# Optimization experiments

Hardware: AMD Instinct MI355X
Metric: run time of the kernel (lower is better)

Reference implementation:

```python
import jax, jax.numpy as jnp
import numpy as np

D_MODEL = 1024
NUM_HEADS = 16
D_K = D_MODEL // NUM_HEADS
B, S = 2, 2048


def setup_inputs() -> dict:
    key = jax.random.key(0)
    ks = jax.random.split(key, 9)
    scale = 1.0 / np.sqrt(D_MODEL)
    return {
        "hidden_states": jax.random.normal(ks[0], (B, S, D_MODEL), dtype=jnp.float32),
        "attention_mask": jnp.ones((B, S, S), dtype=jnp.int32),
        "Wq": jax.random.normal(ks[1], (D_MODEL, D_MODEL), dtype=jnp.float32) * scale,
        "bq": jnp.zeros((D_MODEL,), dtype=jnp.float32),
        "Wk": jax.random.normal(ks[2], (D_MODEL, D_MODEL), dtype=jnp.float32) * scale,
        "bk": jnp.zeros((D_MODEL,), dtype=jnp.float32),
        "Wv": jax.random.normal(ks[3], (D_MODEL, D_MODEL), dtype=jnp.float32) * scale,
        "bv": jnp.zeros((D_MODEL,), dtype=jnp.float32),
        "Wo": jax.random.normal(ks[4], (D_MODEL, D_MODEL), dtype=jnp.float32) * scale,
        "bo": jnp.zeros((D_MODEL,), dtype=jnp.float32),
    }


def reference(hidden_states, attention_mask, Wq, bq, Wk, bk, Wv, bv, Wo, bo):
    b, s, _ = hidden_states.shape
    # torch Linear: y = x @ W.T + b
    def proj(W, bias):
        y = jnp.einsum('bsd,ed->bse', hidden_states, W) + bias
        return y.reshape(b, s, NUM_HEADS, D_K).transpose(0, 2, 1, 3)  # [B,H,S,dk]
    q = proj(Wq, bq)
    k = proj(Wk, bk)
    v = proj(Wv, bv)
    scores = jnp.einsum('bnqd,bnkd->bnqk', q, k) / np.sqrt(D_K)
    mask = attention_mask[:, None, :, :]  # [B,1,S,S]
    scores = jnp.where(mask == 0, jnp.float32(-1e9), scores)
    attn = jax.nn.softmax(scores, axis=-1)  # dropout = identity (eval)
    ctx = jnp.einsum('bnqk,bnkd->bnqd', attn, v)
    ctx = ctx.transpose(0, 2, 1, 3).reshape(b, s, D_MODEL)
    return jnp.einsum('bsd,ed->bse', ctx, Wo) + bo
```

## Files before the change

kernel.cpp:

```cpp
#include <hip/hip_runtime.h>

typedef short short8 __attribute__((ext_vector_type(8)));
typedef float floatx4 __attribute__((ext_vector_type(4)));
typedef float floatx16 __attribute__((ext_vector_type(16)));
typedef unsigned short ushort4v __attribute__((ext_vector_type(4)));

#define DEV static __device__ __forceinline__

DEV unsigned short f2bf(float f) {
  unsigned int u = __builtin_bit_cast(unsigned int, f);
  u += 0x7fffu + ((u >> 16) & 1u);
  return (unsigned short)(u >> 16);
}

DEV unsigned int cvtpk(float a, float b) {
  unsigned int r;
  asm("v_cvt_pk_bf16_f32 %0, %1, %2" : "=v"(r) : "v"(a), "v"(b));
  return r;
}

DEV void gload16(const unsigned short* g, unsigned short* l) {
  __builtin_amdgcn_global_load_lds((__attribute__((address_space(1))) void*)g,
                                   (__attribute__((address_space(3))) void*)l,
                                   16, 0, 0);
}

__global__ void convert_kernel(const float* __restrict__ hs, const float* __restrict__ Wq,
                               const float* __restrict__ Wk, const float* __restrict__ Wv,
                               const float* __restrict__ Wo,
                               unsigned short* __restrict__ xbf, unsigned short* __restrict__ wqkv,
                               unsigned short* __restrict__ wobf,
                               const int* __restrict__ mask, unsigned long long* __restrict__ bits) {
  if (blockIdx.x >= 8192) {
    int w = (blockIdx.x - 8192) * 256 + threadIdx.x;
    const int4* p = (const int4*)(mask + (size_t)w * 64);
    unsigned long long r = 0ull;
#pragma unroll
    for (int j = 0; j < 16; ++j) {
      int4 m = p[j];
      r |= (unsigned long long)(m.x != 0) << (j * 4 + 0);
      r |= (unsigned long long)(m.y != 0) << (j * 4 + 1);
      r |= (unsigned long long)(m.z != 0) << (j * 4 + 2);
      r |= (unsigned long long)(m.w != 0) << (j * 4 + 3);
    }
    bits[w] = r;
    return;
  }
  size_t i4 = ((size_t)blockIdx.x * 256 + threadIdx.x) * 4;
  const float* src;
  unsigned short* dst;
  if (i4 < 4194304) {
    const int r = (int)(i4 >> 10), c = (int)(i4 & 1023);
    src = hs + i4;
    const int p = r >> 6, fi = (r & 63) >> 4, l15f = r & 15;
    const int ktc = c >> 5, qdc = (c >> 3) & 3, e = c & 7;
    dst = xbf + ((size_t)(p * 128 + ktc * 4 + fi) * 512 + (qdc * 16 + l15f) * 8 + e);
  } else if (i4 < 7340032) {
    size_t o = i4 - 4194304;
    size_t lo = o & 1048575;
    src = (o < 1048576) ? (Wq + lo) : ((o < 2097152) ? (Wk + lo) : (Wv + lo));
    const int r = (int)(o >> 10), c = (int)(o & 1023);
    const int p = r >> 6, fi = (r & 63) >> 4, l15f = r & 15;
    const int ktc = c >> 5, qdc = (c >> 3) & 3, e = c & 7;
    dst = wqkv + ((size_t)(p * 128 + ktc * 4 + fi) * 512 + (qdc * 16 + l15f) * 8 + e);
  } else {
    size_t o = i4 - 7340032;
    src = Wo + o; dst = wobf + o;
  }
  float4 v = *(const float4*)src;
  ushort4v u;
  u.x = f2bf(v.x); u.y = f2bf(v.y); u.z = f2bf(v.z); u.w = f2bf(v.w);
  *(ushort4v*)dst = u;
}

__global__ void __launch_bounds__(256, 2) qkv_gemm(
    const unsigned short* __restrict__ Xf, const unsigned short* __restrict__ Wf,
    const float* __restrict__ bq, const float* __restrict__ bk, const float* __restrict__ bv,
    unsigned short* __restrict__ Qb, unsigned short* __restrict__ Kb,
    unsigned short* __restrict__ Vt) {
  const int tid = threadIdx.x;
  const int lane = tid & 63, wv = tid >> 6;
  const int wm = wv >> 1, wn = wv & 1;
  const int quad = lane >> 4, l15 = lane & 15;
  const int mb = blockIdx.y, nb = blockIdx.x;
  const bool sw = (nb < 16);

  const int wx = sw ? wn : wm;
  const int ww = sw ? wm : wn;

  const unsigned short* xp = Xf + (size_t)(mb * 2 + wx) * 65536 + lane * 8;
  const unsigned short* wp = Wf + (size_t)(nb * 2 + ww) * 65536 + lane * 8;

  short8 xa[4], wb[4];
#pragma unroll
  for (int i = 0; i < 4; ++i) xa[i] = *(const short8*)(xp + i * 512);
#pragma unroll
  for (int i = 0; i < 4; ++i) wb[i] = *(const short8*)(wp + i * 512);

  floatx4 acc[4][4] = {};
  for (int kt = 0; kt < 32; ++kt) {
    if (sw) {
#pragma unroll
      for (int mt = 0; mt < 4; ++mt)
#pragma unroll
        for (int nt = 0; nt < 4; ++nt)
          acc[mt][nt] = __builtin_amdgcn_mfma_f32_16x16x32_bf16(wb[mt], xa[nt], acc[mt][nt], 0, 0, 0);
    } else {
#pragma unroll
      for (int mt = 0; mt < 4; ++mt)
#pragma unroll
        for (int nt = 0; nt < 4; ++nt)
          acc[mt][nt] = __builtin_amdgcn_mfma_f32_16x16x32_bf16(xa[mt], wb[nt], acc[mt][nt], 0, 0, 0);
    }
    xp += 2048; wp += 2048;
    if (kt < 31) {
#pragma unroll
      for (int i = 0; i < 4; ++i) xa[i] = *(const short8*)(xp + i * 512);
#pragma unroll
      for (int i = 0; i < 4; ++i) wb[i] = *(const short8*)(wp + i * 512);
    }
  }

  if (sw) {
#pragma unroll
    for (int mt = 0; mt < 4; ++mt) {
      const int wc0 = nb * 128 + wm * 64 + mt * 16 + quad * 4;
      const int mat = wc0 >> 10;
      const int nl0 = wc0 & 1023;
      const int hh = nl0 >> 6, d0 = nl0 & 63;
      const float4 b4 = *(const float4*)((mat ? bk : bq) + nl0);
      const float fac = mat ? 1.0f : 0.18033688011112042f;
#pragma unroll
      for (int nt = 0; nt < 4; ++nt) {
        const int colx = mb * 128 + wn * 64 + nt * 16 + l15;
        const int bb = colx >> 11, s = colx & 2047;
        ushort4v pv;
        pv[0] = f2bf((acc[mt][nt][0] + b4.x) * fac);
        pv[1] = f2bf((acc[mt][nt][1] + b4.y) * fac);
        pv[2] = f2bf((acc[mt][nt][2] + b4.z) * fac);
        pv[3] = f2bf((acc[mt][nt][3] + b4.w) * fac);
        if (mat == 0) {
          *(ushort4v*)&Qb[((size_t)(bb * 16 + hh) * 2048 + s) * 64 + d0] = pv;
        } else {
          const size_t idx = (size_t)(bb * 16 + hh) * 131072 + (s >> 5) * 2048 +
                             (d0 >> 4) * 512 + (((d0 >> 3) & 1) * 32 + (s & 31)) * 8 + (d0 & 7);
          *(ushort4v*)&Kb[idx] = pv;
        }
      }
    }
  } else {
#pragma unroll
    for (int nt = 0; nt < 4; ++nt) {
      const int col = nb * 128 + wn * 64 + nt * 16 + l15;
      const int nl = col & 1023;
      const float bias = bv[nl];
      const int hh = nl >> 6, d = nl & 63;
#pragma unroll
      for (int mt = 0; mt < 4; ++mt) {
        const int row0 = mb * 128 + wm * 64 + mt * 16 + quad * 4;
        const int bb = row0 >> 11, s0 = row0 & 2047;
        ushort4v pv;
#pragma unroll
        for (int r = 0; r < 4; ++r) pv[r] = f2bf(acc[mt][nt][r] + bias);
        const size_t idx = (size_t)(bb * 16 + hh) * 131072 + (s0 >> 5) * 2048 +
                           ((s0 >> 4) & 1) * 1024 + (d >> 5) * 512 +
                           (((s0 >> 3) & 1) * 32 + (d & 31)) * 8 + (s0 & 7);
        *(ushort4v*)&Vt[idx] = pv;
      }
    }
  }
}

__global__ void __launch_bounds__(256, 2) attn_kernel(
    const unsigned short* __restrict__ Qb, const unsigned short* __restrict__ Kb,
    const unsigned short* __restrict__ Vt, const unsigned long long* __restrict__ mbits,
    unsigned short* __restrict__ ctx) {
  __shared__ float red[2 * 64 * 33];
  const int tid = threadIdx.x;
  const int lane = tid & 63, wv = tid >> 6;
  const int l31 = lane & 31, h = lane >> 5;
  const int qg = wv & 1, h2 = wv >> 1;
  const int bid = (blockIdx.x & 7) * 128 + (blockIdx.x >> 3);
  const int pair = bid >> 5, qt = bid & 31;
  const int b_ = pair >> 4, hd = pair & 15;
  const int qrow = qt * 64 + qg * 32 + l31;

  short8 qf[4];
#pragma unroll
  for (int ks = 0; ks < 4; ++ks)
    qf[ks] = *(const short8*)(Qb + (size_t)pair * 131072 + (size_t)qrow * 64 + ks * 16 + h * 8);

  const unsigned short* kp = Kb + (size_t)pair * 131072 + h2 * 65536 + lane * 8;
  const unsigned short* vp = Vt + (size_t)pair * 131072 + h2 * 65536 + lane * 8;

  const unsigned long long* mrow = mbits + ((size_t)b_ * 2048 + qrow) * 32 + h2 * 16;

  short8 kf[4], vf[4];
#pragma unroll
  for (int i = 0; i < 4; ++i) kf[i] = *(const short8*)(kp + i * 512);
#pragma unroll
  for (int i = 0; i < 4; ++i) vf[i] = *(const short8*)(vp + i * 512);

  floatx16 acc_o[2] = {};
  const floatx16 Zv = {};
  float lsum = 0.f;

#pragma unroll 2
  for (int it = 0; it < 32; ++it) {
    const unsigned long long w = mrow[it >> 1];
    const int bitbase = (it & 1) * 32;

    __builtin_amdgcn_s_setprio(1);
    floatx16 accs = __builtin_amdgcn_mfma_f32_32x32x16_bf16(kf[0], qf[0], Zv, 0, 0, 0);
#pragma unroll
    for (int ks = 1; ks < 4; ++ks)
      accs = __builtin_amdgcn_mfma_f32_32x32x16_bf16(kf[ks], qf[ks], accs, 0, 0, 0);
    __builtin_amdgcn_s_setprio(0);

    kp += 2048;
#pragma unroll
    for (int i = 0; i < 4; ++i) kf[i] = *(const short8*)(kp + i * 512);

    if (__any(w != ~0ull)) {
#pragma unroll
      for (int reg = 0; reg < 16; ++reg) {
        const int kl = (reg & 3) + 8 * (reg >> 2) + 4 * h;
        if (!((w >> (bitbase + kl)) & 1ull)) accs[reg] = -6e9f;
      }
    }

    unsigned int pk[8];
    float ls0 = 0.f, ls1 = 0.f;
#pragma unroll
    for (int i = 0; i < 8; ++i) {
      const float a = exp2f(accs[2 * i]);
      const float b = exp2f(accs[2 * i + 1]);
      ls0 += a;
      ls1 += b;
      pk[i] = cvtpk(a, b);
    }
    lsum += ls0 + ls1;
#pragma unroll
    for (int u = 0; u < 2; ++u) {
      auto r02 = __builtin_amdgcn_permlane32_swap(pk[4 * u + 0], pk[4 * u + 2], false, false);
      auto r13 = __builtin_amdgcn_permlane32_swap(pk[4 * u + 1], pk[4 * u + 3], false, false);
      union { unsigned int wd[4]; short8 s8; } af;
      af.wd[0] = r02[0];
      af.wd[1] = r13[0];
      af.wd[2] = r02[1];
      af.wd[3] = r13[1];
      __builtin_amdgcn_s_setprio(1);
#pragma unroll
      for (int nt = 0; nt < 2; ++nt)
        acc_o[nt] = __builtin_amdgcn_mfma_f32_32x32x16_bf16(af.s8, vf[u * 2 + nt], acc_o[nt], 0, 0, 0);
      __builtin_amdgcn_s_setprio(0);
    }

    vp += 2048;
#pragma unroll
    for (int i = 0; i < 4; ++i) vf[i] = *(const short8*)(vp + i * 512);
  }

  lsum += __shfl_xor(lsum, 32);

  if (h2 == 1) {
    float* p = red + (qg * 64 + lane) * 33;
#pragma unroll
    for (int reg = 0; reg < 16; ++reg) {
      p[reg] = acc_o[0][reg];
      p[16 + reg] = acc_o[1][reg];
    }
    p[32] = lsum;
  }
  __syncthreads();
  if (h2 == 0) {
    const float* p = red + (qg * 64 + lane) * 33;
#pragma unroll
    for (int reg = 0; reg < 16; ++reg) {
      acc_o[0][reg] += p[reg];
      acc_o[1][reg] += p[16 + reg];
    }
    lsum += p[32];
    const float rinv = 1.f / ((lsum > 0.f) ? lsum : 1.f);
#pragma unroll
    for (int reg = 0; reg < 16; ++reg) {
      const int ql = (reg & 3) + 8 * (reg >> 2) + 4 * h;
      const float rl = __shfl(rinv, ql);
      const size_t base = ((size_t)b_ * 2048 + qt * 64 + qg * 32 + ql) * 1024 + hd * 64;
      ctx[base + l31]      = f2bf(acc_o[0][reg] * rl);
      ctx[base + 32 + l31] = f2bf(acc_o[1][reg] * rl);
    }
  }
}

__global__ void __launch_bounds__(256, 2) out_gemm(
    const unsigned short* __restrict__ C, const unsigned short* __restrict__ W,
    const float* __restrict__ bo, float* __restrict__ out) {
  __shared__ __align__(16) unsigned short As[128 * 32];
  __shared__ __align__(16) unsigned short Bs[64 * 32];
  const int tid = threadIdx.x;
  const int lane = tid & 63, wv = tid >> 6;
  const int wm = wv >> 1, wn = wv & 1;
  const int quad = lane >> 4, l15 = lane & 15;
  const int mb = blockIdx.y, nb = blockIdx.x;

  const unsigned short* ga = C + (size_t)(mb * 128 + (tid >> 2)) * 1024 + (tid & 3) * 8;
  const unsigned short* gb = W + (size_t)(nb * 64 + (tid >> 2)) * 1024 + (tid & 3) * 8;
  unsigned short* la1 = As + tid * 8;
  unsigned short* la2 = As + 2048 + tid * 8;
  unsigned short* lb1 = Bs + tid * 8;

  floatx4 acc[4][2] = {};
  for (int kt = 0; kt < 32; ++kt) {
    const int k0 = kt * 32;
    gload16(ga + k0, la1);
    gload16(ga + k0 + 65536, la2);
    gload16(gb + k0, lb1);
    __syncthreads();
    short8 af[4], bfr[2];
#pragma unroll
    for (int i = 0; i < 4; ++i)
      af[i] = *(const short8*)&As[(wm * 64 + i * 16 + l15) * 32 + quad * 8];
#pragma unroll
    for (int i = 0; i < 2; ++i)
      bfr[i] = *(const short8*)&Bs[(wn * 32 + i * 16 + l15) * 32 + quad * 8];
#pragma unroll
    for (int mt = 0; mt < 4; ++mt)
#pragma unroll
      for (int nt = 0; nt < 2; ++nt)
        acc[mt][nt] = __builtin_amdgcn_mfma_f32_16x16x32_bf16(af[mt], bfr[nt], acc[mt][nt], 0, 0, 0);
    __syncthreads();
  }
#pragma unroll
  for (int nt = 0; nt < 2; ++nt) {
    const int col = nb * 64 + wn * 32 + nt * 16 + l15;
    const float bias = bo[col];
#pragma unroll
    for (int mt = 0; mt < 4; ++mt)
#pragma unroll
      for (int r = 0; r < 4; ++r) {
        const int row = mb * 128 + wm * 64 + mt * 16 + quad * 4 + r;
        out[(size_t)row * 1024 + col] = acc[mt][nt][r] + bias;
      }
  }
}

extern "C" void kernel_launch(void* const* d_in, const int* in_sizes, int n_in,
                              void* d_out, int out_size, void* d_ws, size_t ws_size,
                              hipStream_t stream) {
  const float* hs = (const float*)d_in[0];
  const int* mask = (const int*)d_in[1];
  const float* Wq = (const float*)d_in[2];
  const float* bq = (const float*)d_in[3];
  const float* Wk = (const float*)d_in[4];
  const float* bk = (const float*)d_in[5];
  const float* Wv = (const float*)d_in[6];
  const float* bv = (const float*)d_in[7];
  const float* Wo = (const float*)d_in[8];
  const float* bo = (const float*)d_in[9];
  float* out = (float*)d_out;

  char* ws = (char*)d_ws;
  unsigned short* xbf  = (unsigned short*)(ws + 0);
  unsigned short* wqkv = (unsigned short*)(ws + 8388608);
  unsigned short* wobf = (unsigned short*)(ws + 14680064);
  unsigned short* Qb   = (unsigned short*)(ws + 16777216);
  unsigned short* Kb   = (unsigned short*)(ws + 25165824);
  unsigned short* Vt   = (unsigned short*)(ws + 33554432);
  unsigned short* ctx  = (unsigned short*)(ws + 41943040);
  unsigned long long* mbits = (unsigned long long*)(ws + 50331648);

  convert_kernel<<<8704, 256, 0, stream>>>(hs, Wq, Wk, Wv, Wo, xbf, wqkv, wobf, mask, mbits);
  qkv_gemm<<<dim3(24, 32), 256, 0, stream>>>(xbf, wqkv, bq, bk, bv, Qb, Kb, Vt);
  attn_kernel<<<1024, 256, 0, stream>>>(Qb, Kb, Vt, mbits, ctx);
  out_gemm<<<dim3(16, 32), 256, 0, stream>>>(ctx, wobf, bo, out);
}
```

Baseline: 246.8 us.

## Store ctx and Wo in MFMA fragment layout; load out_gemm operands directly to registers

```diff
diff --git a/kernel.cpp b/kernel.cpp
--- a/kernel.cpp
+++ b/kernel.cpp
@@ -19,11 +19,6 @@
   return r;
 }
 
-DEV void gload16(const unsigned short* g, unsigned short* l) {
-  __builtin_amdgcn_global_load_lds((__attribute__((address_space(1))) void*)g,
-                                   (__attribute__((address_space(3))) void*)l,
-                                   16, 0, 0);
-}
 
 __global__ void convert_kernel(const float* __restrict__ hs, const float* __restrict__ Wq,
                                const float* __restrict__ Wk, const float* __restrict__ Wv,
@@ -49,24 +44,27 @@
   size_t i4 = ((size_t)blockIdx.x * 256 + threadIdx.x) * 4;
   const float* src;
   unsigned short* dst;
+  int r, c;
+  unsigned short* base;
   if (i4 < 4194304) {
-    const int r = (int)(i4 >> 10), c = (int)(i4 & 1023);
     src = hs + i4;
-    const int p = r >> 6, fi = (r & 63) >> 4, l15f = r & 15;
-    const int ktc = c >> 5, qdc = (c >> 3) & 3, e = c & 7;
-    dst = xbf + ((size_t)(p * 128 + ktc * 4 + fi) * 512 + (qdc * 16 + l15f) * 8 + e);
+    r = (int)(i4 >> 10); c = (int)(i4 & 1023);
+    base = xbf;
   } else if (i4 < 7340032) {
     size_t o = i4 - 4194304;
     size_t lo = o & 1048575;
     src = (o < 1048576) ? (Wq + lo) : ((o < 2097152) ? (Wk + lo) : (Wv + lo));
-    const int r = (int)(o >> 10), c = (int)(o & 1023);
-    const int p = r >> 6, fi = (r & 63) >> 4, l15f = r & 15;
-    const int ktc = c >> 5, qdc = (c >> 3) & 3, e = c & 7;
-    dst = wqkv + ((size_t)(p * 128 + ktc * 4 + fi) * 512 + (qdc * 16 + l15f) * 8 + e);
+    r = (int)(o >> 10); c = (int)(o & 1023);
+    base = wqkv;
   } else {
     size_t o = i4 - 7340032;
-    src = Wo + o; dst = wobf + o;
-  }
+    src = Wo + o;
+    r = (int)(o >> 10); c = (int)(o & 1023);
+    base = wobf;
+  }
+  const int p = r >> 6, fi = (r & 63) >> 4, l15f = r & 15;
+  const int ktc = c >> 5, qdc = (c >> 3) & 3, e = c & 7;
+  dst = base + ((size_t)(p * 128 + ktc * 4 + fi) * 512 + (qdc * 16 + l15f) * 8 + e);
   float4 v = *(const float4*)src;
   ushort4v u;
   u.x = f2bf(v.x); u.y = f2bf(v.y); u.z = f2bf(v.z); u.w = f2bf(v.w);
@@ -174,7 +172,7 @@
 __global__ void __launch_bounds__(256, 2) attn_kernel(
     const unsigned short* __restrict__ Qb, const unsigned short* __restrict__ Kb,
     const unsigned short* __restrict__ Vt, const unsigned long long* __restrict__ mbits,
-    unsigned short* __restrict__ ctx) {
+    unsigned short* __restrict__ ctxf) {
   __shared__ float red[2 * 64 * 33];
   const int tid = threadIdx.x;
   const int lane = tid & 63, wv = tid >> 6;
@@ -282,54 +280,53 @@
     }
     lsum += p[32];
     const float rinv = 1.f / ((lsum > 0.f) ? lsum : 1.f);
+    const size_t pbaseF = (size_t)(b_ * 32 + qt) * 65536;
+    const int qde = ((l31 >> 3) & 3) * 16;
+    const int e7 = l31 & 7;
 #pragma unroll
     for (int reg = 0; reg < 16; ++reg) {
       const int ql = (reg & 3) + 8 * (reg >> 2) + 4 * h;
       const float rl = __shfl(rinv, ql);
-      const size_t base = ((size_t)b_ * 2048 + qt * 64 + qg * 32 + ql) * 1024 + hd * 64;
-      ctx[base + l31]      = f2bf(acc_o[0][reg] * rl);
-      ctx[base + 32 + l31] = f2bf(acc_o[1][reg] * rl);
+      const int iq = qg * 2 + (ql >> 4);
+      const size_t off = (size_t)(qde + (ql & 15)) * 8 + e7;
+      ctxf[pbaseF + (size_t)((hd * 2) * 4 + iq) * 512 + off]     = f2bf(acc_o[0][reg] * rl);
+      ctxf[pbaseF + (size_t)((hd * 2 + 1) * 4 + iq) * 512 + off] = f2bf(acc_o[1][reg] * rl);
     }
   }
 }
 
 __global__ void __launch_bounds__(256, 2) out_gemm(
-    const unsigned short* __restrict__ C, const unsigned short* __restrict__ W,
+    const unsigned short* __restrict__ Cf, const unsigned short* __restrict__ Wof,
     const float* __restrict__ bo, float* __restrict__ out) {
-  __shared__ __align__(16) unsigned short As[128 * 32];
-  __shared__ __align__(16) unsigned short Bs[64 * 32];
   const int tid = threadIdx.x;
   const int lane = tid & 63, wv = tid >> 6;
   const int wm = wv >> 1, wn = wv & 1;
   const int quad = lane >> 4, l15 = lane & 15;
   const int mb = blockIdx.y, nb = blockIdx.x;
 
-  const unsigned short* ga = C + (size_t)(mb * 128 + (tid >> 2)) * 1024 + (tid & 3) * 8;
-  const unsigned short* gb = W + (size_t)(nb * 64 + (tid >> 2)) * 1024 + (tid & 3) * 8;
-  unsigned short* la1 = As + tid * 8;
-  unsigned short* la2 = As + 2048 + tid * 8;
-  unsigned short* lb1 = Bs + tid * 8;
+  const unsigned short* ap = Cf + (size_t)(mb * 2 + wm) * 65536 + lane * 8;
+  const unsigned short* bp = Wof + (size_t)nb * 65536 + (size_t)(wn * 2) * 512 + lane * 8;
+
+  short8 af[4], bfr[2];
+#pragma unroll
+  for (int i = 0; i < 4; ++i) af[i] = *(const short8*)(ap + i * 512);
+#pragma unroll
+  for (int i = 0; i < 2; ++i) bfr[i] = *(const short8*)(bp + i * 512);
 
   floatx4 acc[4][2] = {};
   for (int kt = 0; kt < 32; ++kt) {
-    const int k0 = kt * 32;
-    gload16(ga + k0, la1);
-    gload16(ga + k0 + 65536, la2);
-    gload16(gb + k0, lb1);
-    __syncthreads();
-    short8 af[4], bfr[2];
-#pragma unroll
-    for (int i = 0; i < 4; ++i)
-      af[i] = *(const short8*)&As[(wm * 64 + i * 16 + l15) * 32 + quad * 8];
-#pragma unroll
-    for (int i = 0; i < 2; ++i)
-      bfr[i] = *(const short8*)&Bs[(wn * 32 + i * 16 + l15) * 32 + quad * 8];
 #pragma unroll
     for (int mt = 0; mt < 4; ++mt)
 #pragma unroll
       for (int nt = 0; nt < 2; ++nt)
         acc[mt][nt] = __builtin_amdgcn_mfma_f32_16x16x32_bf16(af[mt], bfr[nt], acc[mt][nt], 0, 0, 0);
-    __syncthreads();
+    ap += 2048; bp += 2048;
+    if (kt < 31) {
+#pragma unroll
+      for (int i = 0; i < 4; ++i) af[i] = *(const short8*)(ap + i * 512);
+#pragma unroll
+      for (int i = 0; i < 2; ++i) bfr[i] = *(const short8*)(bp + i * 512);
+    }
   }
 #pragma unroll
   for (int nt = 0; nt < 2; ++nt) {
@@ -367,11 +364,11 @@
   unsigned short* Qb   = (unsigned short*)(ws + 16777216);
   unsigned short* Kb   = (unsigned short*)(ws + 25165824);
   unsigned short* Vt   = (unsigned short*)(ws + 33554432);
-  unsigned short* ctx  = (unsigned short*)(ws + 41943040);
+  unsigned short* ctxf = (unsigned short*)(ws + 41943040);
   unsigned long long* mbits = (unsigned long long*)(ws + 50331648);
 
   convert_kernel<<<8704, 256, 0, stream>>>(hs, Wq, Wk, Wv, Wo, xbf, wqkv, wobf, mask, mbits);
   qkv_gemm<<<dim3(24, 32), 256, 0, stream>>>(xbf, wqkv, bq, bk, bv, Qb, Kb, Vt);
-  attn_kernel<<<1024, 256, 0, stream>>>(Qb, Kb, Vt, mbits, ctx);
-  out_gemm<<<dim3(16, 32), 256, 0, stream>>>(ctx, wobf, bo, out);
-}
+  attn_kernel<<<1024, 256, 0, stream>>>(Qb, Kb, Vt, mbits, ctxf);
+  out_gemm<<<dim3(16, 32), 256, 0, stream>>>(ctxf, wobf, bo, out);
+}
```

Result: faster. 238.9 us, median of 2 (-3.2%).
